# Kernel optimization log

Hardware: AMD Instinct MI355X
Metric: run time of the kernel (lower is better)

## Reference

```python
import jax, jax.numpy as jnp
import numpy as np

# KWConv2d config: in=256, out=256, k=3, s=1, p=1, groups=1, bias=False
# warehouse: 32 spatial cells of shape [64, 64, 3, 3]; num_fourier_basis=0; temp_value=0
B, CIN, H, W_ = 32, 256, 56, 56
OUT = 256
NUM_CELLS, CO, CI, KH, KW = 32, 64, 64, 3, 3
HIDDEN = 16                 # max(int(256 * 0.0625), 16)
GO, GI, GS = OUT // CO, CIN // CI, 1
M = GO * GI * GS            # num_local_mixture = 16
P = NUM_CELLS + 1           # kw_planes_per_mixture = 33
KWP = P * M                 # kw_planes = 528


def setup_inputs() -> dict:
    key = jax.random.key(0)
    ks = jax.random.split(key, 4)
    s = 0.02
    return {
        "x": jax.random.normal(ks[0], (B, CIN, H, W_), jnp.float32),
        "cells": jax.random.normal(ks[1], (NUM_CELLS, CO, CI, KH, KW), jnp.float32) * s,
        "fc1_w": jax.random.normal(ks[2], (HIDDEN, CIN), jnp.float32) * s,
        "fc1_b": jnp.zeros((HIDDEN,), jnp.float32),
        "ln_g": jnp.ones((HIDDEN,), jnp.float32),
        "ln_b": jnp.zeros((HIDDEN,), jnp.float32),
        "sp_w": jax.random.normal(ks[3], (KWP, HIDDEN), jnp.float32) * s,
        "sp_b": jnp.zeros((KWP,), jnp.float32),
    }


def _attention(x, fc1_w, fc1_b, ln_g, ln_b, sp_w, sp_b):
    # AdaptiveAvgPool1d(1) over flattened spatial dims == global mean
    pooled = x.mean(axis=(2, 3))                      # [B, CIN]
    h = pooled @ fc1_w.T + fc1_b                      # [B, HIDDEN]
    mu = h.mean(-1, keepdims=True)
    var = ((h - mu) ** 2).mean(-1, keepdims=True)
    h = (h - mu) * jax.lax.rsqrt(var + 1e-5) * ln_g + ln_b
    h = jax.nn.relu(h)
    a = h @ sp_w.T + sp_b                             # spatial_head -> [B, KWP]
    a = a.reshape(-1, P)                              # [B*M, P]
    a = a / (jnp.abs(a).sum(axis=1, keepdims=True) + 0.001)  # L1 normalize per mixture
    # temp_value = 0 -> attention unchanged; drop last (zero) column
    return a[:, :-1]                                  # [B*M, NUM_CELLS]


def reference(x, cells, fc1_w, fc1_b, ln_g, ln_b, sp_w, sp_b):
    att = _attention(x, fc1_w, fc1_b, ln_g, ln_b, sp_w, sp_b)  # [B*M, NUM_CELLS]
    w = cells.reshape(NUM_CELLS, -1)                  # [NUM_CELLS, CO*CI*KH*KW]
    agg = att @ w                                     # [B*M, CO*CI*KH*KW]
    agg = agg.reshape(B, GS, GO, GI, CO, CI, KH, KW)
    agg = agg.transpose(0, 2, 4, 3, 5, 1, 6, 7)       # torch permute (0,2,4,3,5,1,6,7)
    agg = agg.reshape(B * OUT, CIN, KH, KW)           # per-sample kernels (groups=1)
    # grouped-conv trick: fold batch into channels, groups = B
    xr = x.reshape(1, B * CIN, H, W_)
    out = jax.lax.conv_general_dilated(
        xr, agg, window_strides=(1, 1), padding=((1, 1), (1, 1)),
        dimension_numbers=("NCHW", "OIHW", "NCHW"), feature_group_count=B)
    return out.reshape(B, OUT, H, W_)
```

## Files before the change

kernel.cpp:

```cpp
#include <hip/hip_runtime.h>
#include <stdint.h>

typedef unsigned short ush;
typedef __bf16   bf16x8 __attribute__((ext_vector_type(8)));
typedef float    f32x4  __attribute__((ext_vector_type(4)));
typedef uint32_t u32x4  __attribute__((ext_vector_type(4)));

union U16B { u32x4 u; bf16x8 b; };
union P8   { ush us[8]; u32x4 v; };

__device__ __forceinline__ ush f2bf(float f) {
    union { float f; uint32_t u; } v; v.f = f;
    uint32_t r = v.u + 0x7FFFu + ((v.u >> 16) & 1u);
    return (ush)(r >> 16);
}

__device__ __forceinline__ void gl_lds16(const ush* g, ush* l) {
    __builtin_amdgcn_global_load_lds(
        (const __attribute__((address_space(1))) uint32_t*)g,
        (__attribute__((address_space(3))) uint32_t*)l, 16, 0, 0);
}

#define HWPX  3136
#define POOL_OFF   58720256UL
#define ATT_OFF    58753024UL
#define WAGG_OFF   58818560UL

__global__ void k_halo(u32x4* __restrict__ xT16, u32x4* __restrict__ pooled16) {
    int i = blockIdx.x * 256 + threadIdx.x;
    int rl = i >> 3, s = i & 7;
    u32x4 z = (u32x4)(0u);
    size_t byte = (size_t)rl * 4096 + (s < 4 ? s * 16 : 3648 + (s - 4) * 16);
    xT16[byte >> 4] = z;
    if (blockIdx.x < 8) pooled16[blockIdx.x * 256 + threadIdx.x] = z;
}

__global__ void k_transpose(const float* __restrict__ x, ush* __restrict__ xT,
                            float* __restrict__ pooled) {
    __shared__ float tile[64][65];
    int blk = blockIdx.x;
    int b   = blk / 196;
    int rem = blk % 196;
    int icg = rem / 49;
    int pxg = rem % 49;
    int t = threadIdx.x;

    {
        int icl  = t >> 2, part = t & 3;
        const float* src = x + (size_t)(b * 256 + icg * 64 + icl) * HWPX + pxg * 64 + part * 16;
        #pragma unroll
        for (int k = 0; k < 4; ++k) {
            f32x4 v = *(const f32x4*)(src + k * 4);
            tile[icl][part * 16 + k * 4 + 0] = v[0];
            tile[icl][part * 16 + k * 4 + 1] = v[1];
            tile[icl][part * 16 + k * 4 + 2] = v[2];
            tile[icl][part * 16 + k * 4 + 3] = v[3];
        }
    }
    __syncthreads();

    if (t < 64) {
        float s = 0.f;
        #pragma unroll 8
        for (int p = 0; p < 64; ++p) s += tile[t][p];
        atomicAdd(pooled + b * 256 + icg * 64 + t, s);
    }

    {
        int pxl = t >> 2, icq = t & 3;
        int px  = pxg * 64 + pxl;
        int row = px / 56;
        int col = px - row * 56;
        int p   = col + 1;
        int xorp = (p >> 1) & 3;
        int icg32   = icg * 2 + (icq >> 1);
        int subbase = (icq & 1) * 2;
        P8 lo, hi;
        #pragma unroll
        for (int m = 0; m < 8; ++m) {
            lo.us[m] = f2bf(tile[icq * 16 + m][pxl]);
            hi.us[m] = f2bf(tile[icq * 16 + 8 + m][pxl]);
        }
        size_t base = (((size_t)(b * 8 + icg32) * 56 + row) * 64 + p) * 32;
        *(u32x4*)(xT + base + (size_t)((subbase ^ xorp) * 8))       = lo.v;
        *(u32x4*)(xT + base + (size_t)(((subbase + 1) ^ xorp) * 8)) = hi.v;
    }
}

__global__ void k_attn(const float* __restrict__ pooled,
                       const float* __restrict__ fc1_w, const float* __restrict__ fc1_b,
                       const float* __restrict__ ln_g,  const float* __restrict__ ln_b,
                       const float* __restrict__ sp_w,  const float* __restrict__ sp_b,
                       float* __restrict__ att) {
    __shared__ float hs[32][16];
    int t = threadIdx.x;
    {
        int b = t >> 4, j = t & 15;
        float acc = 0.f;
        for (int c = 0; c < 256; ++c) acc += pooled[b * 256 + c] * fc1_w[j * 256 + c];
        hs[b][j] = fc1_b[j] + acc * (1.0f / 3136.0f);
    }
    __syncthreads();
    if (t < 32) {
        float mu = 0.f;
        #pragma unroll
        for (int j = 0; j < 16; ++j) mu += hs[t][j];
        mu *= (1.0f / 16.0f);
        float var = 0.f;
        #pragma unroll
        for (int j = 0; j < 16; ++j) { float d = hs[t][j] - mu; var += d * d; }
        var *= (1.0f / 16.0f);
        float inv = rsqrtf(var + 1e-5f);
        #pragma unroll
        for (int j = 0; j < 16; ++j) {
            float v = (hs[t][j] - mu) * inv * ln_g[j] + ln_b[j];
            hs[t][j] = fmaxf(v, 0.f);
        }
    }
    __syncthreads();
    {
        int b = t >> 4, m = t & 15;
        float a[33];
        #pragma unroll 1
        for (int i = 0; i < 33; ++i) {
            int p = m * 33 + i;
            float acc = sp_b[p];
            #pragma unroll
            for (int j = 0; j < 16; ++j) acc += hs[b][j] * sp_w[p * 16 + j];
            a[i] = acc;
        }
        float s = 0.f;
        #pragma unroll
        for (int i = 0; i < 33; ++i) s += fabsf(a[i]);
        float inv = 1.0f / (s + 0.001f);
        #pragma unroll
        for (int c = 0; c < 32; ++c) att[(b * 16 + m) * 32 + c] = a[c] * inv;
    }
}

__global__ void k_agg(const float* __restrict__ cells, const float* __restrict__ att,
                      ush* __restrict__ wagg) {
    __shared__ float at[512];
    int blk = blockIdx.x;
    int b = blk >> 6, co = blk & 63;
    int t = threadIdx.x;
    for (int i = t; i < 512; i += 256) at[i] = att[b * 512 + i];
    __syncthreads();
    int ci = t & 63, gi = t >> 6;
    float acc[4][9];
    #pragma unroll
    for (int g = 0; g < 4; ++g)
        #pragma unroll
        for (int k = 0; k < 9; ++k) acc[g][k] = 0.f;
    for (int c = 0; c < 32; ++c) {
        float a0 = at[(0 + gi) * 32 + c];
        float a1 = at[(4 + gi) * 32 + c];
        float a2 = at[(8 + gi) * 32 + c];
        float a3 = at[(12 + gi) * 32 + c];
        const float* cp = cells + (size_t)c * 36864 + co * 576 + ci * 9;
        #pragma unroll
        for (int k = 0; k < 9; ++k) {
            float cv = cp[k];
            acc[0][k] += a0 * cv; acc[1][k] += a1 * cv;
            acc[2][k] += a2 * cv; acc[3][k] += a3 * cv;
        }
    }
    #pragma unroll
    for (int g = 0; g < 4; ++g)
        #pragma unroll
        for (int k = 0; k < 9; ++k)
            wagg[((size_t)(b * 9 + k) * 256 + g * 64 + co) * 256 + gi * 64 + ci] = f2bf(acc[g][k]);
}

__global__ __launch_bounds__(256, 2) void k_conv(const ush* __restrict__ xT,
                                                 const ush* __restrict__ wagg,
                                                 float* __restrict__ out) {
    __shared__ __align__(16) ush xs[12288];
    __shared__ __align__(16) ush wsh[23040];

    int tid = threadIdx.x;
    int wg  = blockIdx.x;
    int xcd = wg & 7;
    int kk  = wg >> 3;
    int gq  = kk / 14;
    int sp  = kk - gq * 14;
    int g   = gq * 8 + xcd;
    int b   = g >> 2, octile = g & 3;
    int row0 = sp * 4, oc0 = octile * 64;

    int lane = tid & 63, w = tid >> 6;
    int wm = w >> 1, wn = w & 1;
    int l15 = lane & 15, s4 = lane >> 4;

    {
        u32x4 z = (u32x4)(0u);
        #pragma unroll
        for (int i = 0; i < 6; ++i) ((u32x4*)xs)[tid + i * 256] = z;
    }

    int prow[7], pq[7];
    #pragma unroll
    for (int j = 0; j < 7; ++j) {
        int px = wn * 112 + j * 16 + l15;
        prow[j] = px / 56;
        pq[j]   = px - prow[j] * 56;
    }

    unsigned vmask = 0;
    #pragma unroll
    for (int k = 0; k < 6; ++k) {
        int grow = row0 - 1 + k;
        if (grow >= 0 && grow < 56) vmask |= 1u << k;
    }

    const ush* wgl = wagg + (size_t)b * 9 * 65536 + (size_t)(oc0 + (tid >> 2)) * 256 + (tid & 3) * 8;
    ush* wdst = wsh + (tid >> 2) * 40 + (((tid & 3) ^ ((tid >> 2) & 3)) * 8);
    const ush* wrd = wsh + (wm * 32 + l15) * 40 + ((s4 ^ (l15 & 3)) * 8);
    const ush* xb = xT + (size_t)b * 8 * 56 * 2048 + (size_t)tid * 8;

    f32x4 acc[2][7];
    #pragma unroll
    for (int mi = 0; mi < 2; ++mi)
        #pragma unroll
        for (int j = 0; j < 7; ++j) acc[mi][j] = (f32x4)(0.f);

    __syncthreads();

    if ((kk >> 5) & 1) __builtin_amdgcn_s_sleep(32);

    for (int cc = 0; cc < 8; ++cc) {
        U16B wst[9];
        const ush* wcg = wgl + (size_t)cc * 32;
        #pragma unroll
        for (int k = 0; k < 9; ++k) wst[k].u = *(const u32x4*)(wcg + (size_t)k * 65536);
        #pragma unroll
        for (int k = 0; k < 6; ++k)
            if (vmask & (1u << k))
                gl_lds16(xb + (size_t)(cc * 56 + row0 - 1 + k) * 2048, xs + k * 2048 + w * 512);
        #pragma unroll
        for (int k = 0; k < 9; ++k) *(u32x4*)(wdst + k * 2560) = wst[k].u;
        __syncthreads();

        #pragma unroll
        for (int tap = 0; tap < 9; ++tap) {
            const int dy = tap / 3, dx = tap % 3;
            U16B wf0, wf1;
            wf0.u = *(const u32x4*)(wrd + tap * 2560);
            wf1.u = *(const u32x4*)(wrd + tap * 2560 + 16 * 40);
            U16B bx[7];
            #pragma unroll
            for (int j = 0; j < 7; ++j) {
                int q    = pq[j] + dx;
                int slot = s4 ^ ((q >> 1) & 3);
                bx[j].u = *(const u32x4*)(xs + ((prow[j] + dy) * 64 + q) * 32 + slot * 8);
            }
            __builtin_amdgcn_s_setprio(1);
            #pragma unroll
            for (int j = 0; j < 7; ++j) {
                acc[0][j] = __builtin_amdgcn_mfma_f32_16x16x32_bf16(bx[j].b, wf0.b, acc[0][j], 0, 0, 0);
                acc[1][j] = __builtin_amdgcn_mfma_f32_16x16x32_bf16(bx[j].b, wf1.b, acc[1][j], 0, 0, 0);
            }
            __builtin_amdgcn_s_setprio(0);
        }
        __syncthreads();
    }

    int pxbase = row0 * 56 + wn * 112 + s4 * 4;
    #pragma unroll
    for (int mi = 0; mi < 2; ++mi) {
        int oc = oc0 + wm * 32 + mi * 16 + l15;
        float* o = out + (size_t)(b * 256 + oc) * HWPX + pxbase;
        #pragma unroll
        for (int j = 0; j < 7; ++j)
            *(f32x4*)(o + j * 16) = acc[mi][j];
    }
}

extern "C" void kernel_launch(void* const* d_in, const int* in_sizes, int n_in,
                              void* d_out, int out_size, void* d_ws, size_t ws_size,
                              hipStream_t stream) {
    const float* x     = (const float*)d_in[0];
    const float* cells = (const float*)d_in[1];
    const float* fc1_w = (const float*)d_in[2];
    const float* fc1_b = (const float*)d_in[3];
    const float* ln_g  = (const float*)d_in[4];
    const float* ln_b  = (const float*)d_in[5];
    const float* sp_w  = (const float*)d_in[6];
    const float* sp_b  = (const float*)d_in[7];
    float* out = (float*)d_out;

    char* ws = (char*)d_ws;
    ush*   xT     = (ush*)ws;
    float* pooled = (float*)(ws + POOL_OFF);
    float* att    = (float*)(ws + ATT_OFF);
    ush*   wagg   = (ush*)(ws + WAGG_OFF);

    k_halo<<<448, 256, 0, stream>>>((u32x4*)ws, (u32x4*)pooled);
    k_transpose<<<6272, 256, 0, stream>>>(x, xT, pooled);
    k_attn<<<1, 512, 0, stream>>>(pooled, fc1_w, fc1_b, ln_g, ln_b, sp_w, sp_b, att);
    k_agg<<<2048, 256, 0, stream>>>(cells, att, wagg);
    k_conv<<<1792, 256, 0, stream>>>(xT, wagg, out);
}
```

Baseline: 234.4 us.

## Double-buffer conv input tiles and prefetch next chunk weights, fold halo zeroing into transpose

```diff
diff --git a/kernel.cpp b/kernel.cpp
--- a/kernel.cpp
+++ b/kernel.cpp
@@ -9,6 +9,8 @@
 union U16B { u32x4 u; bf16x8 b; };
 union P8   { ush us[8]; u32x4 v; };
 
+template<int V> struct ICx { static constexpr int value = V; };
+
 __device__ __forceinline__ ush f2bf(float f) {
     union { float f; uint32_t u; } v; v.f = f;
     uint32_t r = v.u + 0x7FFFu + ((v.u >> 16) & 1u);
@@ -25,15 +27,6 @@
 #define POOL_OFF   58720256UL
 #define ATT_OFF    58753024UL
 #define WAGG_OFF   58818560UL
-
-__global__ void k_halo(u32x4* __restrict__ xT16, u32x4* __restrict__ pooled16) {
-    int i = blockIdx.x * 256 + threadIdx.x;
-    int rl = i >> 3, s = i & 7;
-    u32x4 z = (u32x4)(0u);
-    size_t byte = (size_t)rl * 4096 + (s < 4 ? s * 16 : 3648 + (s - 4) * 16);
-    xT16[byte >> 4] = z;
-    if (blockIdx.x < 8) pooled16[blockIdx.x * 256 + threadIdx.x] = z;
-}
 
 __global__ void k_transpose(const float* __restrict__ x, ush* __restrict__ xT,
                             float* __restrict__ pooled) {
@@ -57,6 +50,17 @@
             tile[icl][part * 16 + k * 4 + 3] = v[3];
         }
     }
+
+    if (t < 32) {
+        int r = (pxg * 64 + 55) / 56 + (t >> 4);
+        if (r < 56 && r * 56 <= pxg * 64 + 63) {
+            int icg32 = icg * 2 + ((t >> 3) & 1);
+            int colp  = ((t >> 2) & 1) ? 57 : 0;
+            int chunk = t & 3;
+            u32x4 z = (u32x4)(0u);
+            *(u32x4*)(xT + (((size_t)(b * 8 + icg32) * 56 + r) * 64 + colp) * 32 + chunk * 8) = z;
+        }
+    }
     __syncthreads();
 
     if (t < 64) {
@@ -175,8 +179,8 @@
 __global__ __launch_bounds__(256, 2) void k_conv(const ush* __restrict__ xT,
                                                  const ush* __restrict__ wagg,
                                                  float* __restrict__ out) {
-    __shared__ __align__(16) ush xs[12288];
-    __shared__ __align__(16) ush wsh[23040];
+    __shared__ __align__(16) ush xs[2][12288];
+    __shared__ __align__(16) ush wsh[16384];
 
     int tid = threadIdx.x;
     int wg  = blockIdx.x;
@@ -189,13 +193,13 @@
     int row0 = sp * 4, oc0 = octile * 64;
 
     int lane = tid & 63, w = tid >> 6;
-    int wm = w >> 1, wn = w & 1;
+    int wn = w & 1, ocH = w >> 1;
     int l15 = lane & 15, s4 = lane >> 4;
 
     {
         u32x4 z = (u32x4)(0u);
         #pragma unroll
-        for (int i = 0; i < 6; ++i) ((u32x4*)xs)[tid + i * 256] = z;
+        for (int i = 0; i < 12; ++i) ((u32x4*)xs)[tid + i * 256] = z;
     }
 
     int prow[7], pq[7];
@@ -213,9 +217,10 @@
         if (grow >= 0 && grow < 56) vmask |= 1u << k;
     }
 
-    const ush* wgl = wagg + (size_t)b * 9 * 65536 + (size_t)(oc0 + (tid >> 2)) * 256 + (tid & 3) * 8;
-    ush* wdst = wsh + (tid >> 2) * 40 + (((tid & 3) ^ ((tid >> 2) & 3)) * 8);
-    const ush* wrd = wsh + (wm * 32 + l15) * 40 + ((s4 ^ (l15 & 3)) * 8);
+    const ush* wgl  = wagg + (size_t)b * 9 * 65536 + (size_t)(oc0 + (tid >> 2)) * 256 + (tid & 3) * 8;
+    ush*       wdst = wsh + ((size_t)(tid & 3) * 64 + (tid >> 2)) * 8;
+    const ush* wrd  = wsh + ((size_t)s4 * 64 + ocH * 32 + l15) * 8;
+    const ush* w8gl = wagg + (size_t)(b * 9 + 8) * 65536 + (size_t)(oc0 + ocH * 32 + l15) * 256 + s4 * 8;
     const ush* xb = xT + (size_t)b * 8 * 56 * 2048 + (size_t)tid * 8;
 
     f32x4 acc[2][7];
@@ -226,49 +231,93 @@
 
     __syncthreads();
 
-    if ((kk >> 5) & 1) __builtin_amdgcn_s_sleep(32);
-
-    for (int cc = 0; cc < 8; ++cc) {
-        U16B wst[9];
-        const ush* wcg = wgl + (size_t)cc * 32;
-        #pragma unroll
-        for (int k = 0; k < 9; ++k) wst[k].u = *(const u32x4*)(wcg + (size_t)k * 65536);
+    {
+        U16B wpre[8];
+        #pragma unroll
+        for (int k = 0; k < 8; ++k) wpre[k].u = *(const u32x4*)(wgl + (size_t)k * 65536);
         #pragma unroll
         for (int k = 0; k < 6; ++k)
             if (vmask & (1u << k))
-                gl_lds16(xb + (size_t)(cc * 56 + row0 - 1 + k) * 2048, xs + k * 2048 + w * 512);
-        #pragma unroll
-        for (int k = 0; k < 9; ++k) *(u32x4*)(wdst + k * 2560) = wst[k].u;
+                gl_lds16(xb + (size_t)(row0 - 1 + k) * 2048, &xs[0][0] + k * 2048 + w * 512);
         __syncthreads();
-
-        #pragma unroll
-        for (int tap = 0; tap < 9; ++tap) {
+        #pragma unroll
+        for (int k = 0; k < 8; ++k) *(u32x4*)(wdst + k * 2048) = wpre[k].u;
+        __syncthreads();
+    }
+
+    auto chunk_body = [&](auto parc, int cc) {
+        constexpr int PAR = decltype(parc)::value;
+        U16B wf8[2];
+        wf8[0].u = *(const u32x4*)(w8gl + (size_t)cc * 32);
+        wf8[1].u = *(const u32x4*)(w8gl + (size_t)cc * 32 + 4096);
+        U16B wpre[8];
+        bool pre = cc < 7;
+        if (pre) {
+            const ush* wgc = wgl + (size_t)(cc + 1) * 32;
+            #pragma unroll
+            for (int k = 0; k < 8; ++k) wpre[k].u = *(const u32x4*)(wgc + (size_t)k * 65536);
+            ush* xo = &xs[0][0] + (PAR ^ 1) * 12288;
+            #pragma unroll
+            for (int k = 0; k < 6; ++k)
+                if (vmask & (1u << k))
+                    gl_lds16(xb + (size_t)((cc + 1) * 56 + row0 - 1 + k) * 2048,
+                             xo + k * 2048 + w * 512);
+        }
+        const ush* xsb = &xs[0][0] + PAR * 12288;
+        #pragma unroll
+        for (int tap = 0; tap < 8; ++tap) {
             const int dy = tap / 3, dx = tap % 3;
-            U16B wf0, wf1;
-            wf0.u = *(const u32x4*)(wrd + tap * 2560);
-            wf1.u = *(const u32x4*)(wrd + tap * 2560 + 16 * 40);
+            U16B wf[2];
+            wf[0].u = *(const u32x4*)(wrd + tap * 2048);
+            wf[1].u = *(const u32x4*)(wrd + tap * 2048 + 128);
             U16B bx[7];
             #pragma unroll
             for (int j = 0; j < 7; ++j) {
                 int q    = pq[j] + dx;
                 int slot = s4 ^ ((q >> 1) & 3);
-                bx[j].u = *(const u32x4*)(xs + ((prow[j] + dy) * 64 + q) * 32 + slot * 8);
+                bx[j].u = *(const u32x4*)(xsb + ((prow[j] + dy) * 64 + q) * 32 + slot * 8);
             }
             __builtin_amdgcn_s_setprio(1);
             #pragma unroll
             for (int j = 0; j < 7; ++j) {
-                acc[0][j] = __builtin_amdgcn_mfma_f32_16x16x32_bf16(bx[j].b, wf0.b, acc[0][j], 0, 0, 0);
-                acc[1][j] = __builtin_amdgcn_mfma_f32_16x16x32_bf16(bx[j].b, wf1.b, acc[1][j], 0, 0, 0);
+                acc[0][j] = __builtin_amdgcn_mfma_f32_16x16x32_bf16(bx[j].b, wf[0].b, acc[0][j], 0, 0, 0);
+                acc[1][j] = __builtin_amdgcn_mfma_f32_16x16x32_bf16(bx[j].b, wf[1].b, acc[1][j], 0, 0, 0);
             }
             __builtin_amdgcn_s_setprio(0);
         }
+        {
+            U16B bx[7];
+            #pragma unroll
+            for (int j = 0; j < 7; ++j) {
+                int q    = pq[j] + 2;
+                int slot = s4 ^ ((q >> 1) & 3);
+                bx[j].u = *(const u32x4*)(xsb + ((prow[j] + 2) * 64 + q) * 32 + slot * 8);
+            }
+            __builtin_amdgcn_s_setprio(1);
+            #pragma unroll
+            for (int j = 0; j < 7; ++j) {
+                acc[0][j] = __builtin_amdgcn_mfma_f32_16x16x32_bf16(bx[j].b, wf8[0].b, acc[0][j], 0, 0, 0);
+                acc[1][j] = __builtin_amdgcn_mfma_f32_16x16x32_bf16(bx[j].b, wf8[1].b, acc[1][j], 0, 0, 0);
+            }
+            __builtin_amdgcn_s_setprio(0);
+        }
         __syncthreads();
+        if (pre) {
+            #pragma unroll
+            for (int k = 0; k < 8; ++k) *(u32x4*)(wdst + k * 2048) = wpre[k].u;
+            __syncthreads();
+        }
+    };
+
+    for (int c2 = 0; c2 < 8; c2 += 2) {
+        chunk_body(ICx<0>{}, c2);
+        chunk_body(ICx<1>{}, c2 + 1);
     }
 
     int pxbase = row0 * 56 + wn * 112 + s4 * 4;
     #pragma unroll
     for (int mi = 0; mi < 2; ++mi) {
-        int oc = oc0 + wm * 32 + mi * 16 + l15;
+        int oc = oc0 + ocH * 32 + mi * 16 + l15;
         float* o = out + (size_t)(b * 256 + oc) * HWPX + pxbase;
         #pragma unroll
         for (int j = 0; j < 7; ++j)
@@ -295,7 +344,7 @@
     float* att    = (float*)(ws + ATT_OFF);
     ush*   wagg   = (ush*)(ws + WAGG_OFF);
 
-    k_halo<<<448, 256, 0, stream>>>((u32x4*)ws, (u32x4*)pooled);
+    hipMemsetAsync(pooled, 0, 32768, stream);
     k_transpose<<<6272, 256, 0, stream>>>(x, xT, pooled);
     k_attn<<<1, 512, 0, stream>>>(pooled, fc1_w, fc1_b, ln_g, ln_b, sp_w, sp_b, att);
     k_agg<<<2048, 256, 0, stream>>>(cells, att, wagg);
```

Measured after the change: 240.6 us. 2.6% more time.
